# Optimization experiments

Measured on AMD Instinct MI355X. Metric: run time of the kernel, lower is better.

The kernel has to match this reference:

```python
import jax, jax.numpy as jnp
import numpy as np

N_NODES = 50000
N_EDGES = 800000
D_IN = 128
D_OUT = 128


def setup_inputs() -> dict:
    key = jax.random.key(0)
    k1, k2, k3, k4, k5, k6 = jax.random.split(key, 6)
    x = jax.random.normal(k1, (N_NODES, D_IN), dtype=jnp.float32)
    edge_row = jax.random.randint(k2, (N_EDGES,), 0, N_NODES, dtype=jnp.int32)
    edge_col = jax.random.randint(k3, (N_EDGES,), 0, N_NODES, dtype=jnp.int32)
    edge_weight = jax.random.uniform(k4, (N_EDGES,), dtype=jnp.float32)
    W = jax.random.normal(k5, (D_OUT, D_IN), dtype=jnp.float32) * (1.0 / np.sqrt(D_IN))
    b = jax.random.normal(k6, (D_OUT,), dtype=jnp.float32) * 0.01
    return {"x": x, "edge_row": edge_row, "edge_col": edge_col,
            "edge_weight": edge_weight, "W": W, "b": b}


def reference(x, edge_row, edge_col, edge_weight, W, b):
    # SpMM: out[i] = sum_{e: row[e]==i} weight[e] * x[col[e]]
    msgs = edge_weight[:, None] * x[edge_col]            # [E, D_IN]
    agg = jax.ops.segment_sum(msgs, edge_row, num_segments=N_NODES)  # [N, D_IN]
    # nn.Linear: agg @ W.T + b
    return agg @ W.T + b
```

## Files before the change

kernel.cpp:

```cpp
#include <hip/hip_runtime.h>

#define D 128
#define NB_SHIFT 7
#define BKT_NODES 128
#define PB 256
#define MAXB 400
#define BCAP 2560

typedef __attribute__((ext_vector_type(8))) short bf16x8;
typedef __attribute__((ext_vector_type(4))) float f32x4;

__device__ __forceinline__ short f2bf_rne(float f) {
  unsigned u = __float_as_uint(f);
  unsigned r = u + 0x7fffu + ((u >> 16) & 1u);
  return (short)(r >> 16);
}

__device__ __forceinline__ bf16x8 pack_bf16x8(float4 a, float4 b) {
  bf16x8 h;
  h[0] = f2bf_rne(a.x); h[1] = f2bf_rne(a.y);
  h[2] = f2bf_rne(a.z); h[3] = f2bf_rne(a.w);
  h[4] = f2bf_rne(b.x); h[5] = f2bf_rne(b.y);
  h[6] = f2bf_rne(b.z); h[7] = f2bf_rne(b.w);
  return h;
}

__global__ __launch_bounds__(256) void part_gemm_kernel(
    const int* __restrict__ erow, const int* __restrict__ ecol,
    const float* __restrict__ ew, int* __restrict__ gcur,
    int2* __restrict__ swcol,
    const float* __restrict__ x, const float* __restrict__ W,
    ushort* __restrict__ y, int E, int N, int B) {
  if (blockIdx.x < PB) {
    __shared__ int lh[MAXB];
    const int tid = threadIdx.x;
    for (int i = tid; i < B; i += 256) lh[i] = 0;
    __syncthreads();
    const int chunk = (E + PB - 1) / PB;
    const int begin = blockIdx.x * chunk;
    const int end = min(begin + chunk, E);
    for (int e = begin + tid; e < end; e += 256)
      atomicAdd(&lh[erow[e] >> NB_SHIFT], 1);
    __syncthreads();
    for (int i = tid; i < B; i += 256) {
      int v = lh[i];
      lh[i] = i * BCAP + (v ? atomicAdd(&gcur[i], v) : 0);
    }
    __syncthreads();
    for (int e = begin + tid; e < end; e += 256) {
      int r = erow[e];
      int bkt = r >> NB_SHIFT;
      int pos = atomicAdd(&lh[bkt], 1);
      swcol[pos] = make_int2(((r & (BKT_NODES - 1)) << 16) | ecol[e],
                             __float_as_int(ew[e]));
    }
  } else {
    const int tid = threadIdx.x;
    const int wave = tid >> 6, lane = tid & 63;
    const int m_half = wave & 1;
    const int n_half = wave >> 1;
    const int l16 = lane & 15, quad = lane >> 4;

    bf16x8 Bf[4][4];
    const float4* W4 = (const float4*)W;
#pragma unroll
    for (int nt = 0; nt < 4; ++nt) {
      int n = n_half * 64 + nt * 16 + l16;
#pragma unroll
      for (int kb = 0; kb < 4; ++kb) {
        int idx = (n * D + kb * 32 + quad * 8) >> 2;
        Bf[nt][kb] = pack_bf16x8(W4[idx], W4[idx + 1]);
      }
    }

    const float4* x4 = (const float4*)x;
    const int ntiles = (N + 63) >> 6;
    const int gstride = gridDim.x - PB;
    for (int tile = (int)blockIdx.x - PB; tile < ntiles; tile += gstride) {
      const int row0 = tile * 64 + m_half * 32;
      f32x4 acc[2][4];
#pragma unroll
      for (int mt = 0; mt < 2; ++mt)
#pragma unroll
        for (int nt = 0; nt < 4; ++nt)
          acc[mt][nt] = (f32x4){0.f, 0.f, 0.f, 0.f};

#pragma unroll
      for (int kb = 0; kb < 4; ++kb) {
        const int k0 = kb * 32 + quad * 8;
        int m0 = row0 + l16;      if (m0 > N - 1) m0 = N - 1;
        int m1 = row0 + 16 + l16; if (m1 > N - 1) m1 = N - 1;
        int i0 = (m0 * D + k0) >> 2;
        int i1 = (m1 * D + k0) >> 2;
        float4 p0 = x4[i0], q0 = x4[i0 + 1];
        float4 p1 = x4[i1], q1 = x4[i1 + 1];
        bf16x8 a0 = pack_bf16x8(p0, q0);
        bf16x8 a1 = pack_bf16x8(p1, q1);
#pragma unroll
        for (int nt = 0; nt < 4; ++nt) {
          acc[0][nt] = __builtin_amdgcn_mfma_f32_16x16x32_bf16(a0, Bf[nt][kb], acc[0][nt], 0, 0, 0);
          acc[1][nt] = __builtin_amdgcn_mfma_f32_16x16x32_bf16(a1, Bf[nt][kb], acc[1][nt], 0, 0, 0);
        }
      }

#pragma unroll
      for (int mt = 0; mt < 2; ++mt) {
        int rbase = row0 + mt * 16 + quad * 4;
#pragma unroll
        for (int nt = 0; nt < 4; ++nt) {
          int col = n_half * 64 + nt * 16 + l16;
#pragma unroll
          for (int r = 0; r < 4; ++r) {
            int row = rbase + r;
            if (row < N) y[row * D + col] = (ushort)f2bf_rne(acc[mt][nt][r]);
          }
        }
      }
    }
  }
}

__global__ __launch_bounds__(256) void stage2_kernel(
    const int2* __restrict__ swcol, int2* __restrict__ swcol2,
    const int* __restrict__ gcur,
    int* __restrict__ startN, int* __restrict__ cntN, int N) {
  __shared__ int2 ebuf[BCAP];
  __shared__ int nh[BKT_NODES], sc[BKT_NODES], ncur[BKT_NODES];
  const int b = blockIdx.x, tid = threadIdx.x;
  const int s = b * BCAP;
  int c = gcur[b];
  if (c > BCAP) c = BCAP;

  if (tid < BKT_NODES) nh[tid] = 0;
  for (int j = tid; j < c; j += 256) ebuf[j] = swcol[s + j];
  __syncthreads();

  for (int j = tid; j < c; j += 256) atomicAdd(&nh[ebuf[j].x >> 16], 1);
  __syncthreads();

  if (tid < BKT_NODES) sc[tid] = nh[tid];
  __syncthreads();
  for (int off = 1; off < BKT_NODES; off <<= 1) {
    int v = 0;
    if (tid < BKT_NODES && tid >= off) v = sc[tid - off];
    __syncthreads();
    if (tid < BKT_NODES && tid >= off) sc[tid] += v;
    __syncthreads();
  }
  if (tid < BKT_NODES) {
    int excl = sc[tid] - nh[tid];
    ncur[tid] = excl;
    int node = (b << NB_SHIFT) + tid;
    if (node < N) { startN[node] = s + excl; cntN[node] = nh[tid]; }
  }
  __syncthreads();

  for (int j = tid; j < c; j += 256) {
    int2 en = ebuf[j];
    int pos = atomicAdd(&ncur[en.x >> 16], 1);
    swcol2[s + pos] = en;
  }
}

__global__ __launch_bounds__(256) void gather_agg_kernel(
    const ushort* __restrict__ y, const int* __restrict__ startN,
    const int* __restrict__ cntN, const int2* __restrict__ swcol2,
    const float* __restrict__ bias, float* __restrict__ out, int N) {
  const int node = blockIdx.x * 4 + (threadIdx.x >> 6);
  const int lane = threadIdx.x & 63;
  if (node >= N) return;

  const unsigned* __restrict__ y1 = (const unsigned*)y;
  float2 acc = ((const float2*)bias)[lane];

  const int s = startN[node];
  const int t = s + cntN[node];
#pragma unroll 4
  for (int j = s; j < t; ++j) {
    int2 cw = swcol2[j];
    int col = cw.x & 0xFFFF;
    float wg = __int_as_float(cw.y);
    unsigned v = y1[col * 64 + lane];
    float f0 = __uint_as_float(v << 16);
    float f1 = __uint_as_float(v & 0xffff0000u);
    acc.x += wg * f0;
    acc.y += wg * f1;
  }
  ((float2*)out)[(size_t)node * 64 + lane] = acc;
}

extern "C" void kernel_launch(void* const* d_in, const int* in_sizes, int n_in,
                              void* d_out, int out_size, void* d_ws, size_t ws_size,
                              hipStream_t stream) {
  const float* x    = (const float*)d_in[0];
  const int*   erow = (const int*)d_in[1];
  const int*   ecol = (const int*)d_in[2];
  const float* ew   = (const float*)d_in[3];
  const float* W    = (const float*)d_in[4];
  const float* b    = (const float*)d_in[5];
  float* out = (float*)d_out;

  const int N = in_sizes[0] / D;
  const int E = in_sizes[1];
  const int B = (N + BKT_NODES - 1) >> NB_SHIFT;

  char* ws = (char*)d_ws;
  ushort* y      = (ushort*)ws;
  int2*   swcol  = (int2*)(ws + (size_t)N * D * 2);
  int2*   swcol2 = swcol + (size_t)MAXB * BCAP;
  int*    gcur   = (int*)(swcol2 + (size_t)MAXB * BCAP);
  int*    startN = gcur + MAXB;
  int*    cntN   = startN + N;

  hipMemsetAsync(gcur, 0, (size_t)B * sizeof(int), stream);

  const int ntiles = (N + 63) >> 6;
  part_gemm_kernel<<<PB + ntiles, 256, 0, stream>>>(
      erow, ecol, ew, gcur, swcol, x, W, y, E, N, B);

  stage2_kernel<<<B, 256, 0, stream>>>(swcol, swcol2, gcur, startN, cntN, N);

  gather_agg_kernel<<<(N + 3) / 4, 256, 0, stream>>>(
      y, startN, cntN, swcol2, b, out, N);
}
```

Before: 163.3 us.

## Fuse per-node edge sort into gather kernel using LDS-resident sorted edges

Merges the bucket-local counting sort and the aggregation gather into one kernel, keeping the node-sorted edge list in shared memory instead of writing it and per-node offsets back to global memory. Bucket size is halved to 64 nodes so each block holds a smaller edge set and more blocks are launched. This removes a kernel launch and a global scratch round trip, but each wave now serially processes 16 nodes, reducing parallelism relative to one wave per node.

```diff
diff --git a/kernel.cpp b/kernel.cpp
--- a/kernel.cpp
+++ b/kernel.cpp
@@ -1,11 +1,11 @@
 #include <hip/hip_runtime.h>
 
 #define D 128
-#define NB_SHIFT 7
-#define BKT_NODES 128
+#define NB_SHIFT 6
+#define BKT_NODES 64
 #define PB 256
-#define MAXB 400
-#define BCAP 2560
+#define MAXB 800
+#define BCAP 1280
 
 typedef __attribute__((ext_vector_type(8))) short bf16x8;
 typedef __attribute__((ext_vector_type(4))) float f32x4;
@@ -120,11 +120,12 @@
   }
 }
 
-__global__ __launch_bounds__(256) void stage2_kernel(
-    const int2* __restrict__ swcol, int2* __restrict__ swcol2,
-    const int* __restrict__ gcur,
-    int* __restrict__ startN, int* __restrict__ cntN, int N) {
+__global__ __launch_bounds__(256) void gather_s2_kernel(
+    const ushort* __restrict__ y, const int* __restrict__ gcur,
+    const int2* __restrict__ swcol, const float* __restrict__ bias,
+    float* __restrict__ out, int N) {
   __shared__ int2 ebuf[BCAP];
+  __shared__ int2 ebuf2[BCAP];
   __shared__ int nh[BKT_NODES], sc[BKT_NODES], ncur[BKT_NODES];
   const int b = blockIdx.x, tid = threadIdx.x;
   const int s = b * BCAP;
@@ -147,46 +148,37 @@
     if (tid < BKT_NODES && tid >= off) sc[tid] += v;
     __syncthreads();
   }
-  if (tid < BKT_NODES) {
-    int excl = sc[tid] - nh[tid];
-    ncur[tid] = excl;
-    int node = (b << NB_SHIFT) + tid;
-    if (node < N) { startN[node] = s + excl; cntN[node] = nh[tid]; }
-  }
+  if (tid < BKT_NODES) ncur[tid] = sc[tid] - nh[tid];
   __syncthreads();
 
   for (int j = tid; j < c; j += 256) {
     int2 en = ebuf[j];
     int pos = atomicAdd(&ncur[en.x >> 16], 1);
-    swcol2[s + pos] = en;
-  }
-}
-
-__global__ __launch_bounds__(256) void gather_agg_kernel(
-    const ushort* __restrict__ y, const int* __restrict__ startN,
-    const int* __restrict__ cntN, const int2* __restrict__ swcol2,
-    const float* __restrict__ bias, float* __restrict__ out, int N) {
-  const int node = blockIdx.x * 4 + (threadIdx.x >> 6);
-  const int lane = threadIdx.x & 63;
-  if (node >= N) return;
-
+    ebuf2[pos] = en;
+  }
+  __syncthreads();
+
+  const int wave = tid >> 6, lane = tid & 63;
   const unsigned* __restrict__ y1 = (const unsigned*)y;
-  float2 acc = ((const float2*)bias)[lane];
-
-  const int s = startN[node];
-  const int t = s + cntN[node];
+  const float2 bb = ((const float2*)bias)[lane];
+
+  for (int nl = wave * 16; nl < wave * 16 + 16; ++nl) {
+    int node = (b << NB_SHIFT) + nl;
+    if (node >= N) break;
+    const int st = sc[nl] - nh[nl];
+    const int en = sc[nl];
+    float2 acc = bb;
 #pragma unroll 4
-  for (int j = s; j < t; ++j) {
-    int2 cw = swcol2[j];
-    int col = cw.x & 0xFFFF;
-    float wg = __int_as_float(cw.y);
-    unsigned v = y1[col * 64 + lane];
-    float f0 = __uint_as_float(v << 16);
-    float f1 = __uint_as_float(v & 0xffff0000u);
-    acc.x += wg * f0;
-    acc.y += wg * f1;
-  }
-  ((float2*)out)[(size_t)node * 64 + lane] = acc;
+    for (int j = st; j < en; ++j) {
+      int2 cw = ebuf2[j];
+      int col = cw.x & 0xFFFF;
+      float wg = __int_as_float(cw.y);
+      unsigned v = y1[col * 64 + lane];
+      acc.x += wg * __uint_as_float(v << 16);
+      acc.y += wg * __uint_as_float(v & 0xffff0000u);
+    }
+    ((float2*)out)[(size_t)node * 64 + lane] = acc;
+  }
 }
 
 extern "C" void kernel_launch(void* const* d_in, const int* in_sizes, int n_in,
@@ -205,12 +197,9 @@
   const int B = (N + BKT_NODES - 1) >> NB_SHIFT;
 
   char* ws = (char*)d_ws;
-  ushort* y      = (ushort*)ws;
-  int2*   swcol  = (int2*)(ws + (size_t)N * D * 2);
-  int2*   swcol2 = swcol + (size_t)MAXB * BCAP;
-  int*    gcur   = (int*)(swcol2 + (size_t)MAXB * BCAP);
-  int*    startN = gcur + MAXB;
-  int*    cntN   = startN + N;
+  ushort* y     = (ushort*)ws;
+  int2*   swcol = (int2*)(ws + (size_t)N * D * 2);
+  int*    gcur  = (int*)(swcol + (size_t)MAXB * BCAP);
 
   hipMemsetAsync(gcur, 0, (size_t)B * sizeof(int), stream);
 
@@ -218,8 +207,5 @@
   part_gemm_kernel<<<PB + ntiles, 256, 0, stream>>>(
       erow, ecol, ew, gcur, swcol, x, W, y, E, N, B);
 
-  stage2_kernel<<<B, 256, 0, stream>>>(swcol, swcol2, gcur, startN, cntN, N);
-
-  gather_agg_kernel<<<(N + 3) / 4, 256, 0, stream>>>(
-      y, startN, cntN, swcol2, b, out, N);
-}
+  gather_s2_kernel<<<B, 256, 0, stream>>>(y, gcur, swcol, b, out, N);
+}
```

New measurement: 171.4 us. 4.9% more time.
